# Kernel optimization log

Measured on AMD Instinct MI355X. Metric: run time of the kernel, lower is better.

## Reference

```python
import jax, jax.numpy as jnp
import numpy as np

B, T, D, H = 4, 2048, 512, 8
DK = D // H

def setup_inputs() -> dict:
    key = jax.random.key(0)
    ks = jax.random.split(key, 5)
    s = 1.0 / np.sqrt(D)
    return {
        "x": jax.random.normal(ks[0], (B, T, D), dtype=jnp.float32),
        "Wq": jax.random.normal(ks[1], (D, D), dtype=jnp.float32) * s,
        "bq": jnp.zeros((D,), dtype=jnp.float32),
        "Wk": jax.random.normal(ks[2], (D, D), dtype=jnp.float32) * s,
        "bk": jnp.zeros((D,), dtype=jnp.float32),
        "Wv": jax.random.normal(ks[3], (D, D), dtype=jnp.float32) * s,
        "bv": jnp.zeros((D,), dtype=jnp.float32),
        "Wo": jax.random.normal(ks[4], (D, D), dtype=jnp.float32) * s,
        "bo": jnp.zeros((D,), dtype=jnp.float32),
    }

def reference(x, Wq, bq, Wk, bk, Wv, bv, Wo, bo):
    # Linear projections (torch Linear: x @ W.T + b); split into heads.
    q = (x @ Wq.T + bq).reshape(B, T, H, DK)  # [B,T,H,dk]
    k = (x @ Wk.T + bk).reshape(B, T, H, DK)
    v = (x @ Wv.T + bv).reshape(B, T, H, DK)
    scale = 1.0 / np.sqrt(DK)
    # scores: [B,H,T,T]
    scores = jnp.einsum("bqhd,bkhd->bhqk", q, k) * scale
    attn = jax.nn.softmax(scores, axis=-1)
    ctx = jnp.einsum("bhqk,bkhd->bqhd", attn, v).reshape(B, T, D)
    return ctx @ Wo.T + bo
```

## Files before the change

### kernel.cpp

```cpp
#include <hip/hip_runtime.h>
#include <stdint.h>

#define NB 4
#define NT 2048
#define ND 512
#define NH 8
#define NDK 64
#define NM (NB*NT)

typedef __attribute__((ext_vector_type(8))) short short8;
typedef __attribute__((ext_vector_type(4))) short bs4;
typedef __attribute__((ext_vector_type(4))) float f32x4;

__device__ __forceinline__ unsigned short f2b(float f) {
    union { float f; uint32_t u; } v; v.f = f;
    return (unsigned short)((v.u + 0x7FFFu + ((v.u >> 16) & 1u)) >> 16);
}

__device__ __forceinline__ void load_lds16(const void* g, void* l) {
    void* gn = const_cast<void*>(g);
    __builtin_amdgcn_global_load_lds((__attribute__((address_space(1))) void*)gn,
                                     (__attribute__((address_space(3))) void*)l,
                                     16, 0, 0);
}

__global__ void convert_all(const float* __restrict__ x,  const float* __restrict__ wq,
                            const float* __restrict__ wk, const float* __restrict__ wv,
                            const float* __restrict__ wo, unsigned short* __restrict__ dst) {
    size_t i = ((size_t)blockIdx.x * 256 + threadIdx.x) * 4;
    const float* src; size_t off;
    if (i < 4194304) { src = x; off = i; }
    else {
        size_t j = i - 4194304;
        src = (j < 262144) ? wq : (j < 524288) ? wk : (j < 786432) ? wv : wo;
        off = j & 262143;
    }
    f32x4 v = *(const f32x4*)(src + off);
    ushort4 r;
    r.x = f2b(v[0]); r.y = f2b(v[1]); r.z = f2b(v[2]); r.w = f2b(v[3]);
    *(ushort4*)(dst + i) = r;
}

__global__ __launch_bounds__(256, 3) void proj_gemm(
        const unsigned short* __restrict__ X,
        const unsigned short* __restrict__ Wbase,
        const float* __restrict__ bias0, const float* __restrict__ bias1,
        const float* __restrict__ bias2,
        unsigned short* __restrict__ Obase, unsigned short* __restrict__ VTb,
        float scale0) {
    const int z = blockIdx.z;
    const float* bias = (z == 0) ? bias0 : (z == 1 ? bias1 : bias2);
    const float scale = (z == 0) ? scale0 : 1.0f;

    int rowBase, colBase;
    const unsigned short *Ap, *Bp;
    if (z == 2) {
        rowBase = blockIdx.x * 128;  colBase = blockIdx.y * 128;
        Ap = Wbase + 2 * (ND * ND);  Bp = X;
    } else {
        rowBase = blockIdx.y * 128;  colBase = blockIdx.x * 128;
        Ap = X;                      Bp = Wbase + (size_t)z * (ND * ND);
    }

    __shared__ alignas(16) unsigned short ldsA[128 * 32];
    __shared__ alignas(16) unsigned short ldsW[128 * 32];

    const int tid = threadIdx.x;
    const int lane = tid & 63, wave = tid >> 6;
    const int quad = lane >> 4, l15 = lane & 15;
    const int wm = wave >> 1, wn = wave & 1;

    const int rS = wave * 16 + (lane >> 2);
    const int kS = (lane & 3) * 8;
    const unsigned short* gA = Ap + (size_t)(rowBase + rS) * ND + kS;
    const unsigned short* gW = Bp + (size_t)(colBase + rS) * ND + kS;
    unsigned short* lA = ldsA + wave * 512;
    unsigned short* lW = ldsW + wave * 512;

    f32x4 acc[4][4];
#pragma unroll
    for (int i = 0; i < 4; i++)
#pragma unroll
        for (int j = 0; j < 4; j++) acc[i][j] = (f32x4)0.0f;

    for (int kt = 0; kt < ND / 32; ++kt) {
        __syncthreads();
        load_lds16(gA,            lA);
        load_lds16(gA + 64 * ND,  lA + 2048);
        load_lds16(gW,            lW);
        load_lds16(gW + 64 * ND,  lW + 2048);
        gA += 32; gW += 32;
        __syncthreads();

        short8 af[4], bfm[4];
#pragma unroll
        for (int mt = 0; mt < 4; ++mt)
            af[mt] = *(const short8*)(ldsA + (wm * 64 + mt * 16 + l15) * 32 + quad * 8);
#pragma unroll
        for (int nt = 0; nt < 4; ++nt)
            bfm[nt] = *(const short8*)(ldsW + (wn * 64 + nt * 16 + l15) * 32 + quad * 8);
#pragma unroll
        for (int mt = 0; mt < 4; ++mt)
#pragma unroll
            for (int nt = 0; nt < 4; ++nt)
                acc[mt][nt] = __builtin_amdgcn_mfma_f32_16x16x32_bf16(
                    af[mt], bfm[nt], acc[mt][nt], 0, 0, 0);
    }

    if (z == 2) {
        const int bz = colBase >> 11;
        const int t0 = colBase & 2047;
        unsigned short* VTo = VTb + ((size_t)(bz * 512 + rowBase)) * NT + t0;
#pragma unroll
        for (int mt = 0; mt < 4; mt++)
#pragma unroll
            for (int reg = 0; reg < 4; reg++) {
                int m = wm * 64 + mt * 16 + quad * 4 + reg;
                float bm = bias[rowBase + m];
                unsigned short* dst = VTo + (size_t)m * NT + wn * 64 + l15;
#pragma unroll
                for (int nt = 0; nt < 4; nt++)
                    dst[nt * 16] = f2b(acc[mt][nt][reg] + bm);
            }
    } else {
        float biasr[4];
#pragma unroll
        for (int nt = 0; nt < 4; nt++)
            biasr[nt] = bias[colBase + wn * 64 + nt * 16 + l15];
        unsigned short* Oz = Obase + (size_t)z * ((size_t)NM * ND);
#pragma unroll
        for (int mt = 0; mt < 4; mt++) {
            int row = rowBase + wm * 64 + mt * 16 + quad * 4;
#pragma unroll
            for (int reg = 0; reg < 4; reg++) {
                unsigned short* dst = Oz + (size_t)(row + reg) * ND + colBase + wn * 64 + l15;
#pragma unroll
                for (int nt = 0; nt < 4; nt++)
                    dst[nt * 16] = f2b((acc[mt][nt][reg] + biasr[nt]) * scale);
            }
        }
    }
}

__global__ __launch_bounds__(256, 4) void out_gemm(
        const unsigned short* __restrict__ A, const unsigned short* __restrict__ W,
        const float* __restrict__ bias, float* __restrict__ OF) {
    __shared__ alignas(16) unsigned short ldsA[64 * 32];
    __shared__ alignas(16) unsigned short ldsW[128 * 32];

    const int tid = threadIdx.x;
    const int lane = tid & 63, wave = tid >> 6;
    const int quad = lane >> 4, l15 = lane & 15;
    const int wm = wave >> 1, wn = wave & 1;
    const int rowBase = blockIdx.y * 64;
    const int colBase = blockIdx.x * 128;

    const int rW = wave * 16 + (lane >> 2);
    const int kS = (lane & 3) * 8;
    const unsigned short* gA = A + (size_t)(rowBase + rW) * ND + kS;
    const unsigned short* gW = W + (size_t)(colBase + rW) * ND + kS;
    unsigned short* lA = ldsA + wave * 512;
    unsigned short* lW = ldsW + wave * 512;

    f32x4 acc[2][4];
#pragma unroll
    for (int mt = 0; mt < 2; mt++)
#pragma unroll
        for (int nt = 0; nt < 4; nt++) acc[mt][nt] = (f32x4)0.0f;

    for (int kt = 0; kt < ND / 32; ++kt) {
        __syncthreads();
        load_lds16(gA,           lA);
        load_lds16(gW,           lW);
        load_lds16(gW + 64 * ND, lW + 2048);
        gA += 32; gW += 32;
        __syncthreads();

        short8 af[2], bfm[4];
#pragma unroll
        for (int mt = 0; mt < 2; ++mt)
            af[mt] = *(const short8*)(ldsA + (wm * 32 + mt * 16 + l15) * 32 + quad * 8);
#pragma unroll
        for (int nt = 0; nt < 4; ++nt)
            bfm[nt] = *(const short8*)(ldsW + (wn * 64 + nt * 16 + l15) * 32 + quad * 8);
#pragma unroll
        for (int mt = 0; mt < 2; ++mt)
#pragma unroll
            for (int nt = 0; nt < 4; ++nt)
                acc[mt][nt] = __builtin_amdgcn_mfma_f32_16x16x32_bf16(
                    af[mt], bfm[nt], acc[mt][nt], 0, 0, 0);
    }

    float biasr[4];
#pragma unroll
    for (int nt = 0; nt < 4; nt++)
        biasr[nt] = bias[colBase + wn * 64 + nt * 16 + l15];

#pragma unroll
    for (int mt = 0; mt < 2; mt++)
#pragma unroll
        for (int reg = 0; reg < 4; reg++) {
            int row = rowBase + wm * 32 + mt * 16 + quad * 4 + reg;
            float* dst = OF + (size_t)row * ND + colBase + wn * 64 + l15;
#pragma unroll
            for (int nt = 0; nt < 4; nt++)
                dst[nt * 16] = acc[mt][nt][reg] + biasr[nt];
        }
}

__global__ __launch_bounds__(256, 4) void attn_kernel(
        const unsigned short* __restrict__ Qb, const unsigned short* __restrict__ Kb,
        const unsigned short* __restrict__ VTb, unsigned short* __restrict__ Cb) {
    const int qt = blockIdx.x, h = blockIdx.y, b = blockIdx.z;
    __shared__ alignas(16) unsigned short Ks[2 * 64 * 64];
    __shared__ alignas(16) unsigned short Vt[2 * 64 * 64];

    const int tid = threadIdx.x, lane = tid & 63, wave = tid >> 6;
    const int quad = lane >> 4, l15 = lane & 15;
    const size_t headOff = (size_t)h * NDK;
    const size_t rowB = (size_t)b * NT;
    const unsigned short* VT = VTb + (size_t)(b * NH + h) * ((size_t)NDK * NT);

    short8 aq[2];
#pragma unroll
    for (int ks = 0; ks < 2; ++ks)
        aq[ks] = *(const short8*)(Qb + (rowB + qt * 64 + wave * 16 + l15) * ND
                                  + headOff + ks * 32 + quad * 8);

    const int r0 = wave * 16 + (lane >> 3);
    const int g0 = (lane & 7) ^ (r0 & 7);
    const unsigned short* Kbh = Kb + rowB * ND + headOff;
    const size_t offK0 = (size_t)r0 * ND + g0 * 8;
    const size_t offK1 = (size_t)(r0 + 8) * ND + g0 * 8;
    const size_t offV0 = (size_t)r0 * NT + g0 * 8;
    const size_t offV1 = (size_t)(r0 + 8) * NT + g0 * 8;

    const int swz = (l15 & 7);

    f32x4 o[4];
#pragma unroll
    for (int nt = 0; nt < 4; nt++) o[nt] = (f32x4)0.0f;
    float lacc = 0.0f;

    {
        unsigned short* dK = Ks + wave * 1024;
        unsigned short* dV = Vt + wave * 1024;
        load_lds16(Kbh + offK0, dK);
        load_lds16(Kbh + offK1, dK + 512);
        load_lds16(VT + offV0, dV);
        load_lds16(VT + offV1, dV + 512);
    }

    for (int kv = 0; kv < NT / 64; ++kv) {
        __syncthreads();

        if (kv + 1 < NT / 64) {
            const unsigned short* kb = Kbh + (size_t)(kv + 1) * 64 * ND;
            const unsigned short* vb = VT + (kv + 1) * 64;
            unsigned short* dK = Ks + ((kv + 1) & 1) * 4096 + wave * 1024;
            unsigned short* dV = Vt + ((kv + 1) & 1) * 4096 + wave * 1024;
            load_lds16(kb + offK0, dK);
            load_lds16(kb + offK1, dK + 512);
            load_lds16(vb + offV0, dV);
            load_lds16(vb + offV1, dV + 512);
        }

        const unsigned short* KsC = Ks + (kv & 1) * 4096;
        const unsigned short* VtC = Vt + (kv & 1) * 4096;

        bs4 pk[4];
#pragma unroll
        for (int kt = 0; kt < 4; ++kt) {
            f32x4 st = (f32x4)0.0f;
#pragma unroll
            for (int ks = 0; ks < 2; ++ks) {
                short8 ak = *(const short8*)&KsC[(kt * 16 + l15) * 64
                                                 + (((ks * 4 + quad) ^ swz) * 8)];
                st = __builtin_amdgcn_mfma_f32_16x16x32_bf16(ak, aq[ks], st, 0, 0, 0);
            }
            float p0 = exp2f(st[0]), p1 = exp2f(st[1]);
            float p2 = exp2f(st[2]), p3 = exp2f(st[3]);
            lacc += (p0 + p1) + (p2 + p3);
            uint32_t lo = __builtin_amdgcn_perm(__float_as_uint(p1), __float_as_uint(p0),
                                                0x07060302u);
            uint32_t hi = __builtin_amdgcn_perm(__float_as_uint(p3), __float_as_uint(p2),
                                                0x07060302u);
            union { uint32_t w[2]; bs4 v; } cvt;
            cvt.w[0] = lo; cvt.w[1] = hi;
            pk[kt] = cvt.v;
        }

#pragma unroll
        for (int kt = 0; kt < 4; ++kt)
#pragma unroll
            for (int nt = 0; nt < 4; ++nt) {
                int cc = kt * 2 + (quad >> 1);
                bs4 vbf = *(const bs4*)&VtC[(nt * 16 + l15) * 64
                                            + ((cc ^ swz) * 8) + (quad & 1) * 4];
                o[nt] = __builtin_amdgcn_mfma_f32_16x16x16bf16_1k(pk[kt], vbf, o[nt], 0, 0, 0);
            }
    }

    lacc += __shfl_xor(lacc, 16);
    lacc += __shfl_xor(lacc, 32);

#pragma unroll
    for (int reg = 0; reg < 4; ++reg) {
        float inv = 1.0f / __shfl(lacc, quad * 4 + reg);
        size_t row = rowB + qt * 64 + wave * 16 + quad * 4 + reg;
#pragma unroll
        for (int nt = 0; nt < 4; ++nt)
            Cb[row * ND + headOff + nt * 16 + l15] = f2b(o[nt][reg] * inv);
    }
}

extern "C" void kernel_launch(void* const* d_in, const int* in_sizes, int n_in,
                              void* d_out, int out_size, void* d_ws, size_t ws_size,
                              hipStream_t stream) {
    (void)in_sizes; (void)n_in; (void)out_size; (void)ws_size;
    const float* x  = (const float*)d_in[0];
    const float* Wq = (const float*)d_in[1];
    const float* bq = (const float*)d_in[2];
    const float* Wk = (const float*)d_in[3];
    const float* bk = (const float*)d_in[4];
    const float* Wv = (const float*)d_in[5];
    const float* bv = (const float*)d_in[6];
    const float* Wo = (const float*)d_in[7];
    const float* bo = (const float*)d_in[8];
    float* out = (float*)d_out;

    unsigned short* ws  = (unsigned short*)d_ws;
    unsigned short* xb  = ws;
    unsigned short* wqb = xb + 4194304;
    unsigned short* Qb  = wqb + 4 * 262144;
    unsigned short* Kb  = Qb + 4194304;
    unsigned short* VTb = Kb + 4194304;
    unsigned short* Cb  = VTb + 4194304;
    unsigned short* wob = wqb + 3 * 262144;

    convert_all<<<5120, 256, 0, stream>>>(x, Wq, Wk, Wv, Wo, ws);

    const float qscale = 0.125f * 1.44269504f;
    proj_gemm<<<dim3(4, 64, 3), 256, 0, stream>>>(xb, wqb, bq, bk, bv, Qb, VTb, qscale);
    attn_kernel<<<dim3(32, 8, 4), 256, 0, stream>>>(Qb, Kb, VTb, Cb);
    out_gemm<<<dim3(4, 128), 256, 0, stream>>>(Cb, wob, bo, out);
}
```

Baseline: 180.4 us.

## Replace double-buffered K/V LDS prefetch with single buffer and precomputed pointers

Removes the double-buffered prefetch of K/V tiles into LDS and instead loads each tile synchronously into a single buffer, bracketed by two barriers per iteration. It also precomputes the swizzled LDS read addresses and the global pointers, which are now incremented each step. Halving LDS use could allow more resident blocks per CU and cuts address arithmetic. The cost is that load latency is no longer hidden behind the MFMA work within a block and there is an extra barrier per iteration.

```diff
diff --git a/kernel.cpp b/kernel.cpp
--- a/kernel.cpp
+++ b/kernel.cpp
@@ -212,8 +212,8 @@
         const unsigned short* __restrict__ Qb, const unsigned short* __restrict__ Kb,
         const unsigned short* __restrict__ VTb, unsigned short* __restrict__ Cb) {
     const int qt = blockIdx.x, h = blockIdx.y, b = blockIdx.z;
-    __shared__ alignas(16) unsigned short Ks[2 * 64 * 64];
-    __shared__ alignas(16) unsigned short Vt[2 * 64 * 64];
+    __shared__ alignas(16) unsigned short Ks[64 * 64];
+    __shared__ alignas(16) unsigned short Vt[64 * 64];
 
     const int tid = threadIdx.x, lane = tid & 63, wave = tid >> 6;
     const int quad = lane >> 4, l15 = lane & 15;
@@ -230,54 +230,44 @@
     const int r0 = wave * 16 + (lane >> 3);
     const int g0 = (lane & 7) ^ (r0 & 7);
     const unsigned short* Kbh = Kb + rowB * ND + headOff;
-    const size_t offK0 = (size_t)r0 * ND + g0 * 8;
-    const size_t offK1 = (size_t)(r0 + 8) * ND + g0 * 8;
-    const size_t offV0 = (size_t)r0 * NT + g0 * 8;
-    const size_t offV1 = (size_t)(r0 + 8) * NT + g0 * 8;
-
-    const int swz = (l15 & 7);
+    const unsigned short* gK0 = Kbh + (size_t)r0 * ND + g0 * 8;
+    const unsigned short* gK1 = Kbh + (size_t)(r0 + 8) * ND + g0 * 8;
+    const unsigned short* gV0 = VT + (size_t)r0 * NT + g0 * 8;
+    const unsigned short* gV1 = VT + (size_t)(r0 + 8) * NT + g0 * 8;
+    unsigned short* ldsK = Ks + wave * 1024;
+    unsigned short* ldsV = Vt + wave * 1024;
+
+    const int swz = l15 & 7;
+    const int qh = quad >> 1, qlo = quad & 1;
+    const unsigned short* kb0 = Ks + l15 * 64 + ((quad ^ swz) * 8);
+    const unsigned short* kb1 = Ks + l15 * 64 + (((4 + quad) ^ swz) * 8);
+    const unsigned short* vbp[4];
+#pragma unroll
+    for (int kt = 0; kt < 4; ++kt)
+        vbp[kt] = Vt + l15 * 64 + (((kt * 2 + qh) ^ swz) * 8) + qlo * 4;
 
     f32x4 o[4];
 #pragma unroll
     for (int nt = 0; nt < 4; nt++) o[nt] = (f32x4)0.0f;
     float lacc = 0.0f;
 
-    {
-        unsigned short* dK = Ks + wave * 1024;
-        unsigned short* dV = Vt + wave * 1024;
-        load_lds16(Kbh + offK0, dK);
-        load_lds16(Kbh + offK1, dK + 512);
-        load_lds16(VT + offV0, dV);
-        load_lds16(VT + offV1, dV + 512);
-    }
-
     for (int kv = 0; kv < NT / 64; ++kv) {
         __syncthreads();
-
-        if (kv + 1 < NT / 64) {
-            const unsigned short* kb = Kbh + (size_t)(kv + 1) * 64 * ND;
-            const unsigned short* vb = VT + (kv + 1) * 64;
-            unsigned short* dK = Ks + ((kv + 1) & 1) * 4096 + wave * 1024;
-            unsigned short* dV = Vt + ((kv + 1) & 1) * 4096 + wave * 1024;
-            load_lds16(kb + offK0, dK);
-            load_lds16(kb + offK1, dK + 512);
-            load_lds16(vb + offV0, dV);
-            load_lds16(vb + offV1, dV + 512);
-        }
-
-        const unsigned short* KsC = Ks + (kv & 1) * 4096;
-        const unsigned short* VtC = Vt + (kv & 1) * 4096;
+        load_lds16(gK0, ldsK);
+        load_lds16(gK1, ldsK + 512);
+        load_lds16(gV0, ldsV);
+        load_lds16(gV1, ldsV + 512);
+        gK0 += 64 * ND; gK1 += 64 * ND; gV0 += 64; gV1 += 64;
+        __syncthreads();
 
         bs4 pk[4];
 #pragma unroll
         for (int kt = 0; kt < 4; ++kt) {
             f32x4 st = (f32x4)0.0f;
-#pragma unroll
-            for (int ks = 0; ks < 2; ++ks) {
-                short8 ak = *(const short8*)&KsC[(kt * 16 + l15) * 64
-                                                 + (((ks * 4 + quad) ^ swz) * 8)];
-                st = __builtin_amdgcn_mfma_f32_16x16x32_bf16(ak, aq[ks], st, 0, 0, 0);
-            }
+            st = __builtin_amdgcn_mfma_f32_16x16x32_bf16(
+                *(const short8*)(kb0 + kt * 1024), aq[0], st, 0, 0, 0);
+            st = __builtin_amdgcn_mfma_f32_16x16x32_bf16(
+                *(const short8*)(kb1 + kt * 1024), aq[1], st, 0, 0, 0);
             float p0 = exp2f(st[0]), p1 = exp2f(st[1]);
             float p2 = exp2f(st[2]), p3 = exp2f(st[3]);
             lacc += (p0 + p1) + (p2 + p3);
@@ -293,12 +283,9 @@
 #pragma unroll
         for (int kt = 0; kt < 4; ++kt)
 #pragma unroll
-            for (int nt = 0; nt < 4; ++nt) {
-                int cc = kt * 2 + (quad >> 1);
-                bs4 vbf = *(const bs4*)&VtC[(nt * 16 + l15) * 64
-                                            + ((cc ^ swz) * 8) + (quad & 1) * 4];
-                o[nt] = __builtin_amdgcn_mfma_f32_16x16x16bf16_1k(pk[kt], vbf, o[nt], 0, 0, 0);
-            }
+            for (int nt = 0; nt < 4; ++nt)
+                o[nt] = __builtin_amdgcn_mfma_f32_16x16x16bf16_1k(
+                    pk[kt], *(const bs4*)(vbp[kt] + nt * 1024), o[nt], 0, 0, 0);
     }
 
     lacc += __shfl_xor(lacc, 16);
```

New measurement: 179.2 us. About the same (-0.7%).
